# Kernel optimization log

Hardware: AMD Instinct MI355X
Metric: run time of the kernel (lower is better)

The kernel has to match this reference:

```python
import jax, jax.numpy as jnp
import numpy as np

N = 100000
E = 3200000
F_IN = 256
HID = 128


def _dconv_k1(x_cat, w, b):
    # torch_geometric_temporal DConv with K=1:
    # H = X @ W[0,0] + X @ W[1,0] + b   (no graph propagation for K=1)
    return x_cat @ (w[0, 0] + w[1, 0]) + b


def _dcrnn_cell(x, h, wz, bz, wr, br, wh, bh):
    xh = jnp.concatenate([x, h], axis=1)
    z = jax.nn.sigmoid(_dconv_k1(xh, wz, bz))
    r = jax.nn.sigmoid(_dconv_k1(xh, wr, br))
    xrh = jnp.concatenate([x, r * h], axis=1)
    h_tilde = jnp.tanh(_dconv_k1(xrh, wh, bh))
    return z * h + (1.0 - z) * h_tilde


def setup_inputs() -> dict:
    key = jax.random.key(0)
    ks = jax.random.split(key, 16)

    def gw(k, shape):
        fan_in = shape[-2]
        return jax.random.normal(k, shape, dtype=jnp.float32) / np.sqrt(fan_in)

    inp = {
        "x": jax.random.normal(ks[0], (N, F_IN), dtype=jnp.float32),
        "edge_index": jax.random.randint(ks[1], (2, E), 0, N, dtype=jnp.int64 if jax.config.jax_enable_x64 else jnp.int32),
        "edge_weight": jax.random.uniform(ks[2], (E,), dtype=jnp.float32),
        "w_z1": gw(ks[3], (2, 1, F_IN + HID, HID)), "b_z1": jnp.zeros((HID,), jnp.float32),
        "w_r1": gw(ks[4], (2, 1, F_IN + HID, HID)), "b_r1": jnp.zeros((HID,), jnp.float32),
        "w_h1": gw(ks[5], (2, 1, F_IN + HID, HID)), "b_h1": jnp.zeros((HID,), jnp.float32),
        "w_z2": gw(ks[6], (2, 1, HID + HID // 2, HID // 2)), "b_z2": jnp.zeros((HID // 2,), jnp.float32),
        "w_r2": gw(ks[7], (2, 1, HID + HID // 2, HID // 2)), "b_r2": jnp.zeros((HID // 2,), jnp.float32),
        "w_h2": gw(ks[8], (2, 1, HID + HID // 2, HID // 2)), "b_h2": jnp.zeros((HID // 2,), jnp.float32),
        "w_lin1": gw(ks[9], (HID // 2, 16)), "b_lin1": jnp.zeros((16,), jnp.float32),
        "w_lin2": gw(ks[10], (16, 1)), "b_lin2": jnp.zeros((1,), jnp.float32),
    }
    return inp


def reference(x, edge_index, edge_weight,
              w_z1, b_z1, w_r1, b_r1, w_h1, b_h1,
              w_z2, b_z2, w_r2, b_r2, w_h2, b_h2,
              w_lin1, b_lin1, w_lin2, b_lin2):
    # edge_index / edge_weight are unused in the K=1 DConv math (faithful to tgt source).
    h0 = jnp.zeros((x.shape[0], w_z1.shape[-1]), x.dtype)
    h = _dcrnn_cell(x, h0, w_z1, b_z1, w_r1, b_r1, w_h1, b_h1)
    h = jax.nn.relu(h)
    h0b = jnp.zeros((x.shape[0], w_z2.shape[-1]), x.dtype)
    h = _dcrnn_cell(h, h0b, w_z2, b_z2, w_r2, b_r2, w_h2, b_h2)
    h = jax.nn.relu(h)
    # Dropout(0.2) is identity at inference
    h = jax.nn.relu(h @ w_lin1 + b_lin1)
    return h @ w_lin2 + b_lin2
```

## Files before the change

### kernel.cpp

```cpp
#include <hip/hip_runtime.h>

typedef _Float16 f16;
typedef _Float16 f16x4 __attribute__((ext_vector_type(4)));
typedef _Float16 f16x8 __attribute__((ext_vector_type(8)));
typedef float    f32x4 __attribute__((ext_vector_type(4)));

#define N_ROWS 100000
#define RT 1563
#define LSX 40
#define LSH1 136
#define LSH2 72

#define W1T_OFF 0
#define W1T_BYTES (256 * 256 * 2)
#define W2T_OFF W1T_BYTES

#define XS0 0
#define XS1 5120
#define WS0 10240
#define WS1 26624
#define ARENA 43008
#define H1S 0
#define H2S 17408

__global__ void prep_w(const float* __restrict__ wz1, const float* __restrict__ wh1,
                       const float* __restrict__ wz2, const float* __restrict__ wh2,
                       f16* __restrict__ W1T, f16* __restrict__ W2T) {
    const int b = blockIdx.x;
    if (b < 256) {
        int idx = b * 256 + threadIdx.x;
        int k = idx >> 8, c = idx & 255;
        const float* w = (c < 128) ? wz1 : wh1;
        int cc = c & 127;
        W1T[c * 256 + k] = (f16)(w[k * 128 + cc] + w[384 * 128 + k * 128 + cc]);
    } else {
        int idx = (b - 256) * 256 + threadIdx.x;
        int k = idx >> 7, c = idx & 127;
        const float* w = (c < 64) ? wz2 : wh2;
        int cc = c & 63;
        W2T[c * 128 + k] = (f16)(w[k * 64 + cc] + w[192 * 64 + k * 64 + cc]);
    }
}

__global__ __launch_bounds__(256, 3) void fused(
    const float* __restrict__ x,
    const f16* __restrict__ W1T, const f16* __restrict__ W2T,
    const float* __restrict__ bz1, const float* __restrict__ bh1,
    const float* __restrict__ bz2, const float* __restrict__ bh2,
    const float* __restrict__ wl1, const float* __restrict__ bl1,
    const float* __restrict__ wl2, const float* __restrict__ bl2,
    float* __restrict__ out)
{
    __shared__ __align__(16) char arena[ARENA];
    const int tid = threadIdx.x, lane = tid & 63, wave = tid >> 6;
    const int ln = lane & 15, quad = lane >> 4;
    const int r0 = blockIdx.x * 64;

    const int xr = tid >> 2, xcg = tid & 3;
    int gxr = r0 + xr; if (gxr >= N_ROWS) gxr = N_ROWS - 1;
    const float* xp = x + (size_t)gxr * 256 + (xcg << 3);
    const int wm = tid >> 4, wn = tid & 15;
    const f16* wp = W1T + (size_t)tid * 256;

    const int Mz = 2 * wave;

    f32x4 acc[4][4];
#pragma unroll
    for (int a = 0; a < 4; ++a)
#pragma unroll
        for (int b = 0; b < 4; ++b) acc[a][b] = (f32x4){0.f, 0.f, 0.f, 0.f};

    float4 pxa, pxb; f16x8 pw[4];
#define PRE(KB) { pxa = *(const float4*)(xp + (KB));  pxb = *(const float4*)(xp + (KB) + 4); \
    _Pragma("unroll") for (int q = 0; q < 4; ++q) pw[q] = *(const f16x8*)(wp + (KB) + (q << 3)); }

    PRE(0)

#pragma unroll
    for (int it = 0; it < 8; ++it) {
        f16* XsB = (f16*)(arena + ((it & 1) ? XS1 : XS0));
        f16* WsB = (f16*)(arena + ((it & 1) ? WS1 : WS0));
        *(f16x8*)&XsB[xr * LSX + (xcg << 3)] =
            (f16x8){(f16)pxa.x,(f16)pxa.y,(f16)pxa.z,(f16)pxa.w,
                    (f16)pxb.x,(f16)pxb.y,(f16)pxb.z,(f16)pxb.w};
#pragma unroll
        for (int q = 0; q < 4; ++q)
            *(f16x8*)&WsB[(wm * 64 + q * 16 + wn) * 8] = pw[q];
        __syncthreads();
        if (it < 7) { PRE((it + 1) * 32) }
        __builtin_amdgcn_sched_barrier(0);

        f16x8 bf[4], af[4];
#pragma unroll
        for (int nt = 0; nt < 4; ++nt)
            bf[nt] = *(const f16x8*)&XsB[(16 * nt + ln) * LSX + quad * 8];
#pragma unroll
        for (int mi = 0; mi < 4; ++mi) {
            const int M = (mi < 2) ? (Mz + mi) : (8 + Mz + mi - 2);
            af[mi] = *(const f16x8*)&WsB[(M * 64 + quad * 16 + ln) * 8];
        }
#pragma unroll
        for (int mi = 0; mi < 4; ++mi)
#pragma unroll
            for (int nt = 0; nt < 4; ++nt)
                acc[mi][nt] = __builtin_amdgcn_mfma_f32_16x16x32_f16(af[mi], bf[nt], acc[mi][nt], 0, 0, 0);
    }
#undef PRE
    __syncthreads();

    f16x8 w2f[2][4];
#pragma unroll
    for (int kc = 0; kc < 4; ++kc) {
        w2f[0][kc] = *(const f16x8*)(W2T + (size_t)(16 * wave + ln) * 128 + kc * 32 + quad * 8);
        w2f[1][kc] = *(const f16x8*)(W2T + (size_t)(64 + 16 * wave + ln) * 128 + kc * 32 + quad * 8);
    }

    f16* h1s = (f16*)(arena + H1S);
#pragma unroll
    for (int mi = 0; mi < 2; ++mi) {
        const int jg0 = 32 * wave + 16 * mi + (quad << 2);
        const float4 zb = *(const float4*)(bz1 + jg0);
        const float4 hb = *(const float4*)(bh1 + jg0);
#pragma unroll
        for (int nt = 0; nt < 4; ++nt) {
            const int row = 16 * nt + ln;
            f16x4 pk;
#pragma unroll
            for (int i = 0; i < 4; ++i) {
                float zp = acc[mi][nt][i]     + (&zb.x)[i];
                float hp = acc[mi + 2][nt][i] + (&hb.x)[i];
                float ex = __expf(2.0f * hp);
                float th = 1.0f - 2.0f / (ex + 1.0f);
                float sg = 1.0f / (1.0f + __expf(zp));
                pk[i] = (f16)fmaxf(th * sg, 0.0f);
            }
            *(f16x4*)&h1s[row * LSH1 + jg0] = pk;
        }
    }
    __syncthreads();

    f32x4 acc2[2][4];
#pragma unroll
    for (int a = 0; a < 2; ++a)
#pragma unroll
        for (int b = 0; b < 4; ++b) acc2[a][b] = (f32x4){0.f, 0.f, 0.f, 0.f};
#pragma unroll
    for (int kc = 0; kc < 4; ++kc) {
        f16x8 bf[4];
#pragma unroll
        for (int nt = 0; nt < 4; ++nt)
            bf[nt] = *(const f16x8*)&h1s[(16 * nt + ln) * LSH1 + kc * 32 + quad * 8];
#pragma unroll
        for (int m = 0; m < 2; ++m)
#pragma unroll
            for (int nt = 0; nt < 4; ++nt)
                acc2[m][nt] = __builtin_amdgcn_mfma_f32_16x16x32_f16(w2f[m][kc], bf[nt], acc2[m][nt], 0, 0, 0);
    }
    __syncthreads();

    f16* h2s = (f16*)(arena + H2S);
    {
        const int jg0 = 16 * wave + (quad << 2);
        const float4 zb = *(const float4*)(bz2 + jg0);
        const float4 hb = *(const float4*)(bh2 + jg0);
#pragma unroll
        for (int nt = 0; nt < 4; ++nt) {
            const int row = 16 * nt + ln;
            f16x4 pk;
#pragma unroll
            for (int i = 0; i < 4; ++i) {
                float zp = acc2[0][nt][i] + (&zb.x)[i];
                float hp = acc2[1][nt][i] + (&hb.x)[i];
                float ex = __expf(2.0f * hp);
                float th = 1.0f - 2.0f / (ex + 1.0f);
                float sg = 1.0f / (1.0f + __expf(zp));
                pk[i] = (f16)fmaxf(th * sg, 0.0f);
            }
            *(f16x4*)&h2s[row * LSH2 + jg0] = pk;
        }
    }
    __syncthreads();

    const float blv = bl1[ln], wlv = wl2[ln], bl2v = bl2[0];
    f16x8 bfr[2];
#pragma unroll
    for (int kc = 0; kc < 2; ++kc)
#pragma unroll
        for (int j = 0; j < 8; ++j)
            bfr[kc][j] = (f16)wl1[(32 * kc + 8 * quad + j) * 16 + ln];

    f32x4 acc3 = (f32x4){0.f, 0.f, 0.f, 0.f};
#pragma unroll
    for (int kc = 0; kc < 2; ++kc) {
        f16x8 af = *(const f16x8*)&h2s[(16 * wave + ln) * LSH2 + kc * 32 + quad * 8];
        acc3 = __builtin_amdgcn_mfma_f32_16x16x32_f16(af, bfr[kc], acc3, 0, 0, 0);
    }
#pragma unroll
    for (int i = 0; i < 4; ++i) {
        float v = fmaxf(acc3[i] + blv, 0.0f) * wlv;
        v += __shfl_xor(v, 1);
        v += __shfl_xor(v, 2);
        v += __shfl_xor(v, 4);
        v += __shfl_xor(v, 8);
        if (ln == 0) {
            const int row = r0 + 16 * wave + (quad << 2) + i;
            if (row < N_ROWS) out[row] = v + bl2v;
        }
    }
}

extern "C" void kernel_launch(void* const* d_in, const int* in_sizes, int n_in,
                              void* d_out, int out_size, void* d_ws, size_t ws_size,
                              hipStream_t stream) {
    const float* x   = (const float*)d_in[0];
    const float* wz1 = (const float*)d_in[3];
    const float* bz1 = (const float*)d_in[4];
    const float* wh1 = (const float*)d_in[7];
    const float* bh1 = (const float*)d_in[8];
    const float* wz2 = (const float*)d_in[9];
    const float* bz2 = (const float*)d_in[10];
    const float* wh2 = (const float*)d_in[13];
    const float* bh2 = (const float*)d_in[14];
    const float* wl1 = (const float*)d_in[15];
    const float* bl1 = (const float*)d_in[16];
    const float* wl2 = (const float*)d_in[17];
    const float* bl2 = (const float*)d_in[18];

    char* ws = (char*)d_ws;
    f16* W1T = (f16*)(ws + W1T_OFF);
    f16* W2T = (f16*)(ws + W2T_OFF);
    float* out = (float*)d_out;

    prep_w<<<320, 256, 0, stream>>>(wz1, wh1, wz2, wh2, W1T, W2T);
    fused<<<RT, 256, 0, stream>>>(x, W1T, W2T, bz1, bh1, bz2, bh2,
                                  wl1, bl1, wl2, bl2, out);
}
```

Before: 240.0 us.

## Stage whole X tile into LDS via global_load_lds and stream weights from registers

Replaces the double-buffered 32-column K loop, which converted X to fp16 and staged both X and W1T through LDS, with one up-front asynchronous global-to-LDS copy of the full 64x256 fp32 X tile. An XOR swizzle is applied to the source addresses to avoid bank conflicts. W1T fragments now go straight from global memory into registers with a one-step software prefetch. This puts many more loads in flight and cuts the per-iteration barriers down to one, aimed at a latency-bound streaming of x. In exchange, LDS use rises to 64KB per block and launch bounds drop to 2 blocks per SM, and the fp32-to-fp16 conversion now happens in the inner loop.

```diff
diff --git a/kernel.cpp b/kernel.cpp
--- a/kernel.cpp
+++ b/kernel.cpp
@@ -7,7 +7,6 @@
 
 #define N_ROWS 100000
 #define RT 1563
-#define LSX 40
 #define LSH1 136
 #define LSH2 72
 
@@ -15,13 +14,10 @@
 #define W1T_BYTES (256 * 256 * 2)
 #define W2T_OFF W1T_BYTES
 
-#define XS0 0
-#define XS1 5120
-#define WS0 10240
-#define WS1 26624
-#define ARENA 43008
-#define H1S 0
-#define H2S 17408
+__device__ __forceinline__ void glds16(const void* g, void* l) {
+    __builtin_amdgcn_global_load_lds((const __attribute__((address_space(1))) void*)g,
+                                     (__attribute__((address_space(3))) void*)l, 16, 0, 0);
+}
 
 __global__ void prep_w(const float* __restrict__ wz1, const float* __restrict__ wh1,
                        const float* __restrict__ wz2, const float* __restrict__ wh2,
@@ -42,7 +38,7 @@
     }
 }
 
-__global__ __launch_bounds__(256, 3) void fused(
+__global__ __launch_bounds__(256, 2) void fused(
     const float* __restrict__ x,
     const f16* __restrict__ W1T, const f16* __restrict__ W2T,
     const float* __restrict__ bz1, const float* __restrict__ bh1,
@@ -51,18 +47,32 @@
     const float* __restrict__ wl2, const float* __restrict__ bl2,
     float* __restrict__ out)
 {
-    __shared__ __align__(16) char arena[ARENA];
+    __shared__ __align__(16) float Xs[64 * 256];
+    f16* h1s = (f16*)Xs;
+    f16* h2s = (f16*)((char*)Xs + 17408);
+
     const int tid = threadIdx.x, lane = tid & 63, wave = tid >> 6;
     const int ln = lane & 15, quad = lane >> 4;
     const int r0 = blockIdx.x * 64;
 
-    const int xr = tid >> 2, xcg = tid & 3;
-    int gxr = r0 + xr; if (gxr >= N_ROWS) gxr = N_ROWS - 1;
-    const float* xp = x + (size_t)gxr * 256 + (xcg << 3);
-    const int wm = tid >> 4, wn = tid & 15;
-    const f16* wp = W1T + (size_t)tid * 256;
-
-    const int Mz = 2 * wave;
+#pragma unroll
+    for (int t = 0; t < 16; ++t) {
+        const int r = wave * 16 + t;
+        int gr = r0 + r; if (gr >= N_ROWS) gr = N_ROWS - 1;
+        glds16(x + (size_t)gr * 256 + (((lane ^ r) & 63) << 2), &Xs[r * 256]);
+    }
+
+    const f16* wbase[4];
+#pragma unroll
+    for (int mi = 0; mi < 4; ++mi) {
+        const int M = (mi < 2) ? (2 * wave + mi) : (8 + 2 * wave + mi - 2);
+        wbase[mi] = W1T + (size_t)(M * 16 + ln) * 256 + quad * 8;
+    }
+    f16x8 wc[4], wn[4];
+#pragma unroll
+    for (int mi = 0; mi < 4; ++mi) wc[mi] = *(const f16x8*)(wbase[mi]);
+
+    __syncthreads();
 
     f32x4 acc[4][4];
 #pragma unroll
@@ -70,42 +80,29 @@
 #pragma unroll
         for (int b = 0; b < 4; ++b) acc[a][b] = (f32x4){0.f, 0.f, 0.f, 0.f};
 
-    float4 pxa, pxb; f16x8 pw[4];
-#define PRE(KB) { pxa = *(const float4*)(xp + (KB));  pxb = *(const float4*)(xp + (KB) + 4); \
-    _Pragma("unroll") for (int q = 0; q < 4; ++q) pw[q] = *(const f16x8*)(wp + (KB) + (q << 3)); }
-
-    PRE(0)
-
-#pragma unroll
-    for (int it = 0; it < 8; ++it) {
-        f16* XsB = (f16*)(arena + ((it & 1) ? XS1 : XS0));
-        f16* WsB = (f16*)(arena + ((it & 1) ? WS1 : WS0));
-        *(f16x8*)&XsB[xr * LSX + (xcg << 3)] =
-            (f16x8){(f16)pxa.x,(f16)pxa.y,(f16)pxa.z,(f16)pxa.w,
-                    (f16)pxb.x,(f16)pxb.y,(f16)pxb.z,(f16)pxb.w};
-#pragma unroll
-        for (int q = 0; q < 4; ++q)
-            *(f16x8*)&WsB[(wm * 64 + q * 16 + wn) * 8] = pw[q];
-        __syncthreads();
-        if (it < 7) { PRE((it + 1) * 32) }
-        __builtin_amdgcn_sched_barrier(0);
-
-        f16x8 bf[4], af[4];
-#pragma unroll
-        for (int nt = 0; nt < 4; ++nt)
-            bf[nt] = *(const f16x8*)&XsB[(16 * nt + ln) * LSX + quad * 8];
-#pragma unroll
-        for (int mi = 0; mi < 4; ++mi) {
-            const int M = (mi < 2) ? (Mz + mi) : (8 + Mz + mi - 2);
-            af[mi] = *(const f16x8*)&WsB[(M * 64 + quad * 16 + ln) * 8];
-        }
+#pragma unroll
+    for (int kc = 0; kc < 8; ++kc) {
 #pragma unroll
         for (int mi = 0; mi < 4; ++mi)
+            wn[mi] = *(const f16x8*)(wbase[mi] + (kc + 1) * 32);
+        f16x8 bf[4];
+#pragma unroll
+        for (int nt = 0; nt < 4; ++nt) {
+            const int row = 16 * nt + ln;
+            const int c0 = kc * 8 + 2 * quad;
+            float4 a = *(const float4*)&Xs[row * 256 + ((c0 ^ row) << 2)];
+            float4 b = *(const float4*)&Xs[row * 256 + (((c0 + 1) ^ row) << 2)];
+            bf[nt] = (f16x8){(f16)a.x,(f16)a.y,(f16)a.z,(f16)a.w,
+                             (f16)b.x,(f16)b.y,(f16)b.z,(f16)b.w};
+        }
+#pragma unroll
+        for (int mi = 0; mi < 4; ++mi)
 #pragma unroll
             for (int nt = 0; nt < 4; ++nt)
-                acc[mi][nt] = __builtin_amdgcn_mfma_f32_16x16x32_f16(af[mi], bf[nt], acc[mi][nt], 0, 0, 0);
-    }
-#undef PRE
+                acc[mi][nt] = __builtin_amdgcn_mfma_f32_16x16x32_f16(wc[mi], bf[nt], acc[mi][nt], 0, 0, 0);
+#pragma unroll
+        for (int mi = 0; mi < 4; ++mi) wc[mi] = wn[mi];
+    }
     __syncthreads();
 
     f16x8 w2f[2][4];
@@ -115,7 +112,6 @@
         w2f[1][kc] = *(const f16x8*)(W2T + (size_t)(64 + 16 * wave + ln) * 128 + kc * 32 + quad * 8);
     }
 
-    f16* h1s = (f16*)(arena + H1S);
 #pragma unroll
     for (int mi = 0; mi < 2; ++mi) {
         const int jg0 = 32 * wave + 16 * mi + (quad << 2);
@@ -158,7 +154,6 @@
     }
     __syncthreads();
 
-    f16* h2s = (f16*)(arena + H2S);
     {
         const int jg0 = 16 * wave + (quad << 2);
         const float4 zb = *(const float4*)(bz2 + jg0);
```

Measured after the change: 244.4 us. Within noise of the previous version (+1.8%).

## Double rows per block to 128 with 512 threads and XOR-swizzled LDS tiles

Applied to the files above, without the earlier changes.

The fused kernel now processes 128 rows per block with 8 waves. Waves are split by output-channel group and by row half, so each staged W1 tile is reused across twice as many rows, roughly halving weight traffic from L2. Padded LDS rows are replaced by an XOR swizzle on the x and weight tiles to avoid bank conflicts. h2 gets its own LDS region, so one barrier can be dropped. The cost is more LDS per block (about 52KB) and a larger block, which may reduce how many blocks fit per CU and leaves only 782 blocks to fill the GPU.

```diff
diff --git a/kernel.cpp b/kernel.cpp
--- a/kernel.cpp
+++ b/kernel.cpp
@@ -6,8 +6,7 @@
 typedef float    f32x4 __attribute__((ext_vector_type(4)));
 
 #define N_ROWS 100000
-#define RT 1563
-#define LSX 40
+#define RT 782
 #define LSH1 136
 #define LSH2 72
 
@@ -16,12 +15,12 @@
 #define W2T_OFF W1T_BYTES
 
 #define XS0 0
-#define XS1 5120
-#define WS0 10240
-#define WS1 26624
-#define ARENA 43008
+#define XS1 8192
+#define WS0 16384
+#define WS1 32768
+#define ARENA 53248
 #define H1S 0
-#define H2S 17408
+#define H2S 34816
 
 __global__ void prep_w(const float* __restrict__ wz1, const float* __restrict__ wh1,
                        const float* __restrict__ wz2, const float* __restrict__ wh2,
@@ -42,7 +41,7 @@
     }
 }
 
-__global__ __launch_bounds__(256, 3) void fused(
+__global__ __launch_bounds__(512, 4) void fused(
     const float* __restrict__ x,
     const f16* __restrict__ W1T, const f16* __restrict__ W2T,
     const float* __restrict__ bz1, const float* __restrict__ bh1,
@@ -54,15 +53,19 @@
     __shared__ __align__(16) char arena[ARENA];
     const int tid = threadIdx.x, lane = tid & 63, wave = tid >> 6;
     const int ln = lane & 15, quad = lane >> 4;
-    const int r0 = blockIdx.x * 64;
-
-    const int xr = tid >> 2, xcg = tid & 3;
+    const int ch = wave >> 1, rh2 = wave & 1;
+    const int r0 = blockIdx.x * 128;
+
+    const int xr = tid >> 2, xg = tid & 3;
+    const int sx = (xr >> 2) & 3;
     int gxr = r0 + xr; if (gxr >= N_ROWS) gxr = N_ROWS - 1;
-    const float* xp = x + (size_t)gxr * 256 + (xcg << 3);
-    const int wm = tid >> 4, wn = tid & 15;
-    const f16* wp = W1T + (size_t)tid * 256;
-
-    const int Mz = 2 * wave;
+    const float* xp = x + (size_t)gxr * 256 + 8 * (xg ^ sx);
+    const int wcl = tid & 255, wp2 = tid >> 8;
+    const int sw = (wcl >> 1) & 3;
+    const f16* wp = W1T + (size_t)wcl * 256;
+    const int wq0 = (2 * wp2) ^ sw, wq1 = (2 * wp2 + 1) ^ sw;
+
+    const int swr = (ln >> 1) & 3;
 
     f32x4 acc[4][4];
 #pragma unroll
@@ -70,9 +73,10 @@
 #pragma unroll
         for (int b = 0; b < 4; ++b) acc[a][b] = (f32x4){0.f, 0.f, 0.f, 0.f};
 
-    float4 pxa, pxb; f16x8 pw[4];
-#define PRE(KB) { pxa = *(const float4*)(xp + (KB));  pxb = *(const float4*)(xp + (KB) + 4); \
-    _Pragma("unroll") for (int q = 0; q < 4; ++q) pw[q] = *(const f16x8*)(wp + (KB) + (q << 3)); }
+    float4 pxa, pxb; f16x8 pw0, pw1;
+#define PRE(R) { pxa = *(const float4*)(xp + (R) * 32);  pxb = *(const float4*)(xp + (R) * 32 + 4); \
+                 pw0 = *(const f16x8*)(wp + (R) * 32 + 8 * wq0); \
+                 pw1 = *(const f16x8*)(wp + (R) * 32 + 8 * wq1); }
 
     PRE(0)
 
@@ -80,24 +84,25 @@
     for (int it = 0; it < 8; ++it) {
         f16* XsB = (f16*)(arena + ((it & 1) ? XS1 : XS0));
         f16* WsB = (f16*)(arena + ((it & 1) ? WS1 : WS0));
-        *(f16x8*)&XsB[xr * LSX + (xcg << 3)] =
+        *(f16x8*)&XsB[xr * 32 + 8 * xg] =
             (f16x8){(f16)pxa.x,(f16)pxa.y,(f16)pxa.z,(f16)pxa.w,
                     (f16)pxb.x,(f16)pxb.y,(f16)pxb.z,(f16)pxb.w};
-#pragma unroll
-        for (int q = 0; q < 4; ++q)
-            *(f16x8*)&WsB[(wm * 64 + q * 16 + wn) * 8] = pw[q];
+        *(f16x8*)&WsB[wcl * 32 + 8 * (2 * wp2)]     = pw0;
+        *(f16x8*)&WsB[wcl * 32 + 8 * (2 * wp2 + 1)] = pw1;
         __syncthreads();
-        if (it < 7) { PRE((it + 1) * 32) }
+        if (it < 7) { PRE(it + 1) }
         __builtin_amdgcn_sched_barrier(0);
 
         f16x8 bf[4], af[4];
 #pragma unroll
-        for (int nt = 0; nt < 4; ++nt)
-            bf[nt] = *(const f16x8*)&XsB[(16 * nt + ln) * LSX + quad * 8];
+        for (int nt = 0; nt < 4; ++nt) {
+            const int row = 64 * rh2 + 16 * nt + ln;
+            bf[nt] = *(const f16x8*)&XsB[row * 32 + 8 * (quad ^ ((row >> 2) & 3))];
+        }
 #pragma unroll
         for (int mi = 0; mi < 4; ++mi) {
-            const int M = (mi < 2) ? (Mz + mi) : (8 + Mz + mi - 2);
-            af[mi] = *(const f16x8*)&WsB[(M * 64 + quad * 16 + ln) * 8];
+            const int M = (mi < 2) ? (2 * ch + mi) : (8 + 2 * ch + mi - 2);
+            af[mi] = *(const f16x8*)&WsB[(M * 16 + ln) * 32 + 8 * (quad ^ swr)];
         }
 #pragma unroll
         for (int mi = 0; mi < 4; ++mi)
@@ -111,19 +116,19 @@
     f16x8 w2f[2][4];
 #pragma unroll
     for (int kc = 0; kc < 4; ++kc) {
-        w2f[0][kc] = *(const f16x8*)(W2T + (size_t)(16 * wave + ln) * 128 + kc * 32 + quad * 8);
-        w2f[1][kc] = *(const f16x8*)(W2T + (size_t)(64 + 16 * wave + ln) * 128 + kc * 32 + quad * 8);
+        w2f[0][kc] = *(const f16x8*)(W2T + (size_t)(16 * ch + ln) * 128 + kc * 32 + quad * 8);
+        w2f[1][kc] = *(const f16x8*)(W2T + (size_t)(64 + 16 * ch + ln) * 128 + kc * 32 + quad * 8);
     }
 
     f16* h1s = (f16*)(arena + H1S);
 #pragma unroll
     for (int mi = 0; mi < 2; ++mi) {
-        const int jg0 = 32 * wave + 16 * mi + (quad << 2);
+        const int jg0 = 32 * ch + 16 * mi + (quad << 2);
         const float4 zb = *(const float4*)(bz1 + jg0);
         const float4 hb = *(const float4*)(bh1 + jg0);
 #pragma unroll
         for (int nt = 0; nt < 4; ++nt) {
-            const int row = 16 * nt + ln;
+            const int row = 64 * rh2 + 16 * nt + ln;
             f16x4 pk;
 #pragma unroll
             for (int i = 0; i < 4; ++i) {
@@ -149,23 +154,22 @@
         f16x8 bf[4];
 #pragma unroll
         for (int nt = 0; nt < 4; ++nt)
-            bf[nt] = *(const f16x8*)&h1s[(16 * nt + ln) * LSH1 + kc * 32 + quad * 8];
+            bf[nt] = *(const f16x8*)&h1s[(64 * rh2 + 16 * nt + ln) * LSH1 + kc * 32 + quad * 8];
 #pragma unroll
         for (int m = 0; m < 2; ++m)
 #pragma unroll
             for (int nt = 0; nt < 4; ++nt)
                 acc2[m][nt] = __builtin_amdgcn_mfma_f32_16x16x32_f16(w2f[m][kc], bf[nt], acc2[m][nt], 0, 0, 0);
     }
-    __syncthreads();
 
     f16* h2s = (f16*)(arena + H2S);
     {
-        const int jg0 = 16 * wave + (quad << 2);
+        const int jg0 = 16 * ch + (quad << 2);
         const float4 zb = *(const float4*)(bz2 + jg0);
         const float4 hb = *(const float4*)(bh2 + jg0);
 #pragma unroll
         for (int nt = 0; nt < 4; ++nt) {
-            const int row = 16 * nt + ln;
+            const int row = 64 * rh2 + 16 * nt + ln;
             f16x4 pk;
 #pragma unroll
             for (int i = 0; i < 4; ++i) {
@@ -232,6 +236,6 @@
     float* out = (float*)d_out;
 
     prep_w<<<320, 256, 0, stream>>>(wz1, wh1, wz2, wh2, W1T, W2T);
-    fused<<<RT, 256, 0, stream>>>(x, W1T, W2T, bz1, bh1, bz2, bh2,
+    fused<<<RT, 512, 0, stream>>>(x, W1T, W2T, bz1, bh1, bz2, bh2,
                                   wl1, bl1, wl2, bl2, out);
 }
```

Result: no change. 243.6 us (+1.5%).
